# Performance work log

Measured on AMD Instinct MI355X. Metric: run time of the kernel, lower is better.

Reference implementation:

```python
import jax, jax.numpy as jnp
import numpy as np

TOP_K = 2

def setup_inputs() -> dict:
    key = jax.random.key(0)
    k1, k2, k3, k4 = jax.random.split(key, 4)
    B, S, H, E, F = 2, 1024, 1024, 16, 1024
    hidden_states = jax.random.normal(k1, (B, S, H), dtype=jnp.float32)
    router_w = jax.random.normal(k2, (H, E), dtype=jnp.float32) * 0.02
    w_gate_up = jax.random.normal(k3, (E, H, 2 * F), dtype=jnp.float32) * 0.02
    w_down = jax.random.normal(k4, (E, F, H), dtype=jnp.float32) * 0.02
    return {"hidden_states": hidden_states, "router_w": router_w,
            "w_gate_up": w_gate_up, "w_down": w_down}

def reference(hidden_states, router_w, w_gate_up, w_down):
    B, S, H = hidden_states.shape
    E = router_w.shape[-1]
    flat = hidden_states.reshape(-1, H)                      # [T, H]
    T = flat.shape[0]
    # Routing: topk_then_softmax (default softmax_order)
    logits = flat @ router_w                                 # [T, E]
    top_vals, top_idx = jax.lax.top_k(logits, TOP_K)         # [T, K]
    routing_weights = jax.nn.softmax(top_vals, axis=-1)      # [T, K]
    # Scatter routing weights into a dense combine matrix [T, E]
    combine = jnp.zeros((T, E), dtype=flat.dtype)
    combine = combine.at[jnp.arange(T)[:, None], top_idx].add(routing_weights)
    # Fused expert FFN (per _FusedExpertTemplate, act_fn = SiLU-gated)
    gu = jnp.einsum('th,ehf->etf', flat, w_gate_up)          # [E, T, 2F]
    gate, up = jnp.split(gu, 2, axis=-1)
    gated = jax.nn.silu(gate) * up                           # [E, T, F]
    expert_out = jnp.einsum('etf,efh->eth', gated, w_down)   # [E, T, H]
    out = jnp.einsum('eth,te->th', expert_out, combine)      # [T, H]
    return out.reshape(B, S, H)
```

## Files before the change

### kernel.cpp

```cpp
#include <hip/hip_runtime.h>

#define T_TOK 2048
#define H_DIM 1024
#define E_NUM 16
#define F_DIM 1024
#define NKB 32

typedef unsigned short u16;
typedef unsigned int u32;
typedef short s16x8 __attribute__((ext_vector_type(8)));
typedef float f32x4 __attribute__((ext_vector_type(4)));

__device__ __forceinline__ float b2f(u16 v) { return __uint_as_float(((u32)v) << 16); }
__device__ __forceinline__ u16 f2b(float f) {
  u32 u = __float_as_uint(f);
  return (u16)((u + 0x7fffu + ((u >> 16) & 1u)) >> 16);
}

__device__ __forceinline__ void gl_lds16(const u32* g, u32* l) {
  __builtin_amdgcn_global_load_lds((const __attribute__((address_space(1))) void*)g,
                                   (__attribute__((address_space(3))) void*)l, 16, 0, 0);
}

__global__ void router_kernel(const float* __restrict__ hidden, const float* __restrict__ rw,
                              int* __restrict__ counts, int* __restrict__ routing_e,
                              float* __restrict__ routing_w) {
  int t = blockIdx.x;
  int lane = threadIdx.x;
  const float* xrow = hidden + (size_t)t * H_DIM;
  float acc[E_NUM];
#pragma unroll
  for (int e = 0; e < E_NUM; ++e) acc[e] = 0.f;
  for (int j = 0; j < H_DIM / 64; ++j) {
    int h = j * 64 + lane;
    float x = xrow[h];
    const float* wr = rw + h * E_NUM;
#pragma unroll
    for (int e = 0; e < E_NUM; ++e) acc[e] += x * wr[e];
  }
#pragma unroll
  for (int e = 0; e < E_NUM; ++e) {
    acc[e] += __shfl_xor(acc[e], 32, 64);
    acc[e] += __shfl_xor(acc[e], 16, 64);
    acc[e] += __shfl_xor(acc[e], 8, 64);
    acc[e] += __shfl_xor(acc[e], 4, 64);
    acc[e] += __shfl_xor(acc[e], 2, 64);
    acc[e] += __shfl_xor(acc[e], 1, 64);
  }
  if (lane == 0) {
    float v0 = -1e30f, v1 = -1e30f;
    int i0 = 0, i1 = 0;
#pragma unroll
    for (int e = 0; e < E_NUM; ++e) {
      float v = acc[e];
      if (v > v0) { v1 = v0; i1 = i0; v0 = v; i0 = e; }
      else if (v > v1) { v1 = v; i1 = e; }
    }
    float p0 = 1.f / (1.f + __expf(v1 - v0));
    routing_e[2 * t] = i0;
    routing_e[2 * t + 1] = i1;
    routing_w[2 * t] = p0;
    routing_w[2 * t + 1] = 1.f - p0;
    atomicAdd(&counts[i0], 1);
    atomicAdd(&counts[i1], 1);
  }
}

__global__ void scatter_kernel(const int* __restrict__ counts, int* __restrict__ offsets,
                               const int* __restrict__ routing_e, const float* __restrict__ routing_w,
                               int* __restrict__ token_of_slot, float* __restrict__ slot_w) {
  __shared__ int offs[E_NUM];
  __shared__ int cur[E_NUM];
  int tid = threadIdx.x;
  if (tid == 0) {
    int s = 0;
    for (int e = 0; e < E_NUM; ++e) { offs[e] = s; s += counts[e]; }
  }
  __syncthreads();
  if (tid < E_NUM) { offsets[tid] = offs[tid]; cur[tid] = offs[tid]; }
  __syncthreads();
  for (int i = tid; i < 2 * T_TOK; i += 256) {
    int e = routing_e[i];
    int pos = atomicAdd(&cur[e], 1);
    token_of_slot[pos] = i >> 1;
    slot_w[pos] = routing_w[i];
  }
}

__device__ __forceinline__ void split_pack(const float* __restrict__ p, uint4& hh, uint4& ll) {
  u16 h[8], l[8];
#pragma unroll
  for (int i = 0; i < 8; ++i) {
    h[i] = f2b(p[i]);
    l[i] = f2b(p[i] - b2f(h[i]));
  }
  hh.x = (u32)h[0] | ((u32)h[1] << 16);
  hh.y = (u32)h[2] | ((u32)h[3] << 16);
  hh.z = (u32)h[4] | ((u32)h[5] << 16);
  hh.w = (u32)h[6] | ((u32)h[7] << 16);
  ll.x = (u32)l[0] | ((u32)l[1] << 16);
  ll.y = (u32)l[2] | ((u32)l[3] << 16);
  ll.z = (u32)l[4] | ((u32)l[5] << 16);
  ll.w = (u32)l[6] | ((u32)l[7] << 16);
}

__global__ __launch_bounds__(256) void prep_x(const float* __restrict__ x, u16* __restrict__ xh,
                                              u16* __restrict__ xl) {
  int i = blockIdx.x * 256 + threadIdx.x;
  float4 a = ((const float4*)x)[2 * i];
  float4 b = ((const float4*)x)[2 * i + 1];
  float v[8] = {a.x, a.y, a.z, a.w, b.x, b.y, b.z, b.w};
  uint4 hh, ll;
  split_pack(v, hh, ll);
  ((uint4*)xh)[i] = hh;
  ((uint4*)xl)[i] = ll;
}

__global__ __launch_bounds__(256) void prep_w(const float* __restrict__ w, u32* __restrict__ wt,
                                              int N) {
  const int e = blockIdx.z, nbk = blockIdx.y, kb = blockIdx.x;
  const float* src = w + (size_t)e * 1024 * N + (size_t)kb * 32 * N + nbk * 128;
  u32* dst = wt + (((size_t)e * gridDim.y + nbk) * NKB + kb) * 2048;
  __shared__ u16 L[32][132];
  const int t = threadIdx.x;
  const int kr = t >> 5;
  const int nq = (t & 31) * 4;
#pragma unroll
  for (int p = 0; p < 4; ++p) {
    int k = p * 8 + kr;
    float4 v = *(const float4*)(src + (size_t)k * N + nq);
    L[k][nq] = f2b(v.x);
    L[k][nq + 1] = f2b(v.y);
    L[k][nq + 2] = f2b(v.z);
    L[k][nq + 3] = f2b(v.w);
  }
  __syncthreads();
  const int n = t >> 1, half = t & 1;
  const int s = ((n >> 3) ^ n) & 3;
  __align__(16) u32 buf[8];
#pragma unroll
  for (int j = 0; j < 8; ++j) {
    int pos = half * 8 + j;
    int g0 = ((pos >> 2) ^ s) & 3;
    int kp = g0 * 4 + (pos & 3);
    buf[j] = (u32)L[2 * kp][n] | ((u32)L[2 * kp + 1][n] << 16);
  }
  *(uint4*)(dst + n * 16 + half * 8) = *(uint4*)&buf[0];
  *(uint4*)(dst + n * 16 + half * 8 + 4) = *(uint4*)&buf[4];
}

__device__ __forceinline__ s16x8 read_bfrag(const u32* __restrict__ B, int n, int q) {
  return *(const s16x8*)&B[n * 16 + (((q ^ (n >> 3) ^ n) & 3) << 2)];
}

#define MFMA(a, b, c) __builtin_amdgcn_mfma_f32_16x16x32_bf16(a, b, c, 0, 0, 0)

__global__ __launch_bounds__(256, 2) void moe_gemm1(
    const u16* __restrict__ Xh, const u16* __restrict__ Xl, const u32* __restrict__ wgu_t,
    const int* __restrict__ token_of_slot, const int* __restrict__ counts,
    const int* __restrict__ offsets, u16* __restrict__ act_h, u16* __restrict__ act_l) {
  const int e = blockIdx.z;
  const int cnt = counts[e];
  const int m0 = blockIdx.y * 64;
  if (m0 >= cnt) return;
  const int off = offsets[e];
  const int xb = blockIdx.x;

  __shared__ u32 Bg[2][2048];
  __shared__ u32 Bu[2][2048];

  const int tid = threadIdx.x;
  const int lane = tid & 63;
  const int wv = tid >> 6;
  const int q = lane >> 4, ln = lane & 15;
  const int mb = (wv & 1) * 32, nb = (wv >> 1) * 64;

  const int r0 = m0 + mb + ln, r1 = r0 + 16;
  const int t0 = (r0 < cnt) ? token_of_slot[off + r0] : 0;
  const int t1 = (r1 < cnt) ? token_of_slot[off + r1] : 0;
  const u16* xh0 = Xh + (size_t)t0 * H_DIM + q * 8;
  const u16* xh1 = Xh + (size_t)t1 * H_DIM + q * 8;
  const u16* xl0 = Xl + (size_t)t0 * H_DIM + q * 8;
  const u16* xl1 = Xl + (size_t)t1 * H_DIM + q * 8;

  const u32* g_g = wgu_t + (((size_t)e * 16 + xb) * NKB) * 2048 + tid * 4;
  const u32* g_u = wgu_t + (((size_t)e * 16 + xb + 8) * NKB) * 2048 + tid * 4;

  f32x4 zero = {0.f, 0.f, 0.f, 0.f};
  f32x4 accg[2][4], accu[2][4];
#pragma unroll
  for (int i = 0; i < 2; ++i)
#pragma unroll
    for (int j = 0; j < 4; ++j) { accg[i][j] = zero; accu[i][j] = zero; }

#define STAGE1(kbn, LG, LU)                          \
  {                                                  \
    const u32* sg = g_g + (size_t)(kbn) * 2048;      \
    const u32* su = g_u + (size_t)(kbn) * 2048;      \
    gl_lds16(sg, (LG) + wv * 256);                   \
    gl_lds16(sg + 1024, (LG) + 1024 + wv * 256);     \
    gl_lds16(su, (LU) + wv * 256);                   \
    gl_lds16(su + 1024, (LU) + 1024 + wv * 256);     \
  }

  STAGE1(0, &Bg[0][0], &Bu[0][0]);
  __syncthreads();

#define G1BODY(kb, CG, CU, NG, NU)                               \
  {                                                              \
    const int koff = (kb) * 32;                                  \
    s16x8 ah0 = *(const s16x8*)(xh0 + koff);                     \
    s16x8 ah1 = *(const s16x8*)(xh1 + koff);                     \
    s16x8 al0 = *(const s16x8*)(xl0 + koff);                     \
    s16x8 al1 = *(const s16x8*)(xl1 + koff);                     \
    if ((kb) + 1 < NKB) STAGE1((kb) + 1, NG, NU);                \
    _Pragma("unroll")                                            \
    for (int j = 0; j < 4; ++j) {                                \
      s16x8 bg = read_bfrag(CG, nb + j * 16 + ln, q);            \
      s16x8 bu = read_bfrag(CU, nb + j * 16 + ln, q);            \
      accg[0][j] = MFMA(ah0, bg, accg[0][j]);                    \
      accg[1][j] = MFMA(ah1, bg, accg[1][j]);                    \
      accu[0][j] = MFMA(ah0, bu, accu[0][j]);                    \
      accu[1][j] = MFMA(ah1, bu, accu[1][j]);                    \
      accg[0][j] = MFMA(al0, bg, accg[0][j]);                    \
      accg[1][j] = MFMA(al1, bg, accg[1][j]);                    \
      accu[0][j] = MFMA(al0, bu, accu[0][j]);                    \
      accu[1][j] = MFMA(al1, bu, accu[1][j]);                    \
    }                                                            \
    __syncthreads();                                             \
  }

  for (int kb = 0; kb < NKB; kb += 2) {
    G1BODY(kb, &Bg[0][0], &Bu[0][0], &Bg[1][0], &Bu[1][0]);
    G1BODY(kb + 1, &Bg[1][0], &Bu[1][0], &Bg[0][0], &Bu[0][0]);
  }

  const int bcol = xb * 128 + nb + ln;
#pragma unroll
  for (int i = 0; i < 2; ++i) {
#pragma unroll
    for (int r = 0; r < 4; ++r) {
      int row = mb + i * 16 + q * 4 + r;
      if (m0 + row < cnt) {
        size_t rb = (size_t)(off + m0 + row) * F_DIM + bcol;
#pragma unroll
        for (int j = 0; j < 4; ++j) {
          float g = accg[i][j][r], u = accu[i][j][r];
          float a = g * (1.f / (1.f + __expf(-g))) * u;
          u16 h = f2b(a);
          u16 l = f2b(a - b2f(h));
          act_h[rb + j * 16] = h;
          act_l[rb + j * 16] = l;
        }
      }
    }
  }
}

__global__ __launch_bounds__(256, 2) void moe_gemm2(
    const u16* __restrict__ Ah, const u16* __restrict__ Al, const u32* __restrict__ wd_t,
    const int* __restrict__ token_of_slot, const float* __restrict__ slot_w,
    const int* __restrict__ counts, const int* __restrict__ offsets,
    float* __restrict__ out) {
  const int e = blockIdx.z;
  const int cnt = counts[e];
  const int m0 = blockIdx.y * 64;
  if (m0 >= cnt) return;
  const int off = offsets[e];
  const int xb = blockIdx.x;

  __shared__ u32 Bd[2][2048];

  const int tid = threadIdx.x;
  const int lane = tid & 63;
  const int wv = tid >> 6;
  const int q = lane >> 4, ln = lane & 15;
  const int mb = (wv & 1) * 32, nb = (wv >> 1) * 64;

  const int r0 = m0 + mb + ln, r1 = r0 + 16;
  const int s0 = off + ((r0 < cnt) ? r0 : 0);
  const int s1 = off + ((r1 < cnt) ? r1 : 0);
  const u16* ah0 = Ah + (size_t)s0 * F_DIM + q * 8;
  const u16* ah1 = Ah + (size_t)s1 * F_DIM + q * 8;
  const u16* al0 = Al + (size_t)s0 * F_DIM + q * 8;
  const u16* al1 = Al + (size_t)s1 * F_DIM + q * 8;

  const u32* g_d = wd_t + (((size_t)e * 8 + xb) * NKB) * 2048 + tid * 4;

  f32x4 zero = {0.f, 0.f, 0.f, 0.f};
  f32x4 acc[2][4];
#pragma unroll
  for (int i = 0; i < 2; ++i)
#pragma unroll
    for (int j = 0; j < 4; ++j) acc[i][j] = zero;

#define STAGE2(kbn, LD)                              \
  {                                                  \
    const u32* sd = g_d + (size_t)(kbn) * 2048;      \
    gl_lds16(sd, (LD) + wv * 256);                   \
    gl_lds16(sd + 1024, (LD) + 1024 + wv * 256);     \
  }

  STAGE2(0, &Bd[0][0]);
  __syncthreads();

#define G2BODY(kb, CD, ND)                               \
  {                                                      \
    const int koff = (kb) * 32;                          \
    s16x8 a0 = *(const s16x8*)(ah0 + koff);              \
    s16x8 a1 = *(const s16x8*)(ah1 + koff);              \
    s16x8 b0 = *(const s16x8*)(al0 + koff);              \
    s16x8 b1 = *(const s16x8*)(al1 + koff);              \
    if ((kb) + 1 < NKB) STAGE2((kb) + 1, ND);            \
    _Pragma("unroll")                                    \
    for (int j = 0; j < 4; ++j) {                        \
      s16x8 bf = read_bfrag(CD, nb + j * 16 + ln, q);    \
      acc[0][j] = MFMA(a0, bf, acc[0][j]);               \
      acc[1][j] = MFMA(a1, bf, acc[1][j]);               \
      acc[0][j] = MFMA(b0, bf, acc[0][j]);               \
      acc[1][j] = MFMA(b1, bf, acc[1][j]);               \
    }                                                    \
    __syncthreads();                                     \
  }

  for (int kb = 0; kb < NKB; kb += 2) {
    G2BODY(kb, &Bd[0][0], &Bd[1][0]);
    G2BODY(kb + 1, &Bd[1][0], &Bd[0][0]);
  }

#pragma unroll
  for (int i = 0; i < 2; ++i) {
#pragma unroll
    for (int r = 0; r < 4; ++r) {
      int row = mb + i * 16 + q * 4 + r;
      if (m0 + row < cnt) {
        int slot = off + m0 + row;
        int tok = token_of_slot[slot];
        float wgt = slot_w[slot];
        float* orow = out + (size_t)tok * H_DIM + xb * 128 + nb + ln;
#pragma unroll
        for (int j = 0; j < 4; ++j) atomicAdd(&orow[j * 16], wgt * acc[i][j][r]);
      }
    }
  }
}

extern "C" void kernel_launch(void* const* d_in, const int* in_sizes, int n_in,
                              void* d_out, int out_size, void* d_ws, size_t ws_size,
                              hipStream_t stream) {
  const float* hidden = (const float*)d_in[0];
  const float* rw = (const float*)d_in[1];
  const float* wgu = (const float*)d_in[2];
  const float* wd = (const float*)d_in[3];
  float* out = (float*)d_out;
  char* ws = (char*)d_ws;

  int* counts = (int*)(ws);
  int* offsets = (int*)(ws + 256);
  int* routing_e = (int*)(ws + 1024);
  float* routing_w = (float*)(ws + 17408);
  int* token_of_slot = (int*)(ws + 33792);
  float* slot_w = (float*)(ws + 50176);
  u16* Xh = (u16*)(ws + 131072ull);
  u16* Xl = (u16*)(ws + 4325376ull);
  u16* act_h = (u16*)(ws + 8519680ull);
  u16* act_l = (u16*)(ws + 16908288ull);
  u32* wgu_t = (u32*)(ws + 25296896ull);
  u32* wd_t  = (u32*)(ws + 92405760ull);

  hipMemsetAsync(counts, 0, 64, stream);
  hipMemsetAsync(out, 0, (size_t)out_size * sizeof(float), stream);
  router_kernel<<<dim3(T_TOK), dim3(64), 0, stream>>>(hidden, rw, counts, routing_e, routing_w);
  scatter_kernel<<<dim3(1), dim3(256), 0, stream>>>(counts, offsets, routing_e, routing_w,
                                                    token_of_slot, slot_w);
  prep_x<<<dim3(T_TOK * H_DIM / 8 / 256), dim3(256), 0, stream>>>(hidden, Xh, Xl);
  prep_w<<<dim3(NKB, 16, E_NUM), dim3(256), 0, stream>>>(wgu, wgu_t, 2048);
  prep_w<<<dim3(NKB, 8, E_NUM), dim3(256), 0, stream>>>(wd, wd_t, 1024);
  moe_gemm1<<<dim3(8, 32, E_NUM), dim3(256), 0, stream>>>(Xh, Xl, wgu_t, token_of_slot, counts,
                                                          offsets, act_h, act_l);
  moe_gemm2<<<dim3(8, 32, E_NUM), dim3(256), 0, stream>>>(act_h, act_l, wd_t, token_of_slot,
                                                          slot_w, counts, offsets, out);
}
```

Before: 479.9 us.

## Deepen GEMM LDS pipelines, prefetch A fragments, restructure router and weight prep

Both expert GEMMs move from a double-buffered LDS pipeline to a four-slot ring with three stages in flight. They use explicit vmcnt waits and raw s_barrier instead of __syncthreads, prefetch the next A fragments into registers, and raise MFMA priority with s_setprio. gemm2 occupancy hint goes to 3 blocks. The router transposes the router weights so each expert's reads coalesce and packs 4 tokens per 256-thread block, and prep_w drops its LDS staging for direct strided column loads. These aim to hide global-load latency and cut barrier stalls, at the cost of more LDS per block (possible occupancy loss in gemm1) and fragile hand-tuned wait counts.

```diff
diff --git a/kernel.cpp b/kernel.cpp
--- a/kernel.cpp
+++ b/kernel.cpp
@@ -22,11 +22,20 @@
                                    (__attribute__((address_space(3))) void*)l, 16, 0, 0);
 }
 
-__global__ void router_kernel(const float* __restrict__ hidden, const float* __restrict__ rw,
-                              int* __restrict__ counts, int* __restrict__ routing_e,
-                              float* __restrict__ routing_w) {
-  int t = blockIdx.x;
-  int lane = threadIdx.x;
+__global__ __launch_bounds__(256) void rw_transpose_kernel(const float* __restrict__ rw,
+                                                           float* __restrict__ rwT) {
+  int idx = blockIdx.x * 256 + threadIdx.x;
+  float v = rw[idx];
+  rwT[(idx & 15) * 1024 + (idx >> 4)] = v;
+}
+
+__global__ __launch_bounds__(256) void router_kernel(const float* __restrict__ hidden,
+                                                     const float* __restrict__ rwT,
+                                                     int* __restrict__ counts,
+                                                     int* __restrict__ routing_e,
+                                                     float* __restrict__ routing_w) {
+  int wv = threadIdx.x >> 6, lane = threadIdx.x & 63;
+  int t = blockIdx.x * 4 + wv;
   const float* xrow = hidden + (size_t)t * H_DIM;
   float acc[E_NUM];
 #pragma unroll
@@ -34,9 +43,8 @@
   for (int j = 0; j < H_DIM / 64; ++j) {
     int h = j * 64 + lane;
     float x = xrow[h];
-    const float* wr = rw + h * E_NUM;
-#pragma unroll
-    for (int e = 0; e < E_NUM; ++e) acc[e] += x * wr[e];
+#pragma unroll
+    for (int e = 0; e < E_NUM; ++e) acc[e] += x * rwT[e * 1024 + h];
   }
 #pragma unroll
   for (int e = 0; e < E_NUM; ++e) {
@@ -121,32 +129,19 @@
   const int e = blockIdx.z, nbk = blockIdx.y, kb = blockIdx.x;
   const float* src = w + (size_t)e * 1024 * N + (size_t)kb * 32 * N + nbk * 128;
   u32* dst = wt + (((size_t)e * gridDim.y + nbk) * NKB + kb) * 2048;
-  __shared__ u16 L[32][132];
   const int t = threadIdx.x;
-  const int kr = t >> 5;
-  const int nq = (t & 31) * 4;
-#pragma unroll
-  for (int p = 0; p < 4; ++p) {
-    int k = p * 8 + kr;
-    float4 v = *(const float4*)(src + (size_t)k * N + nq);
-    L[k][nq] = f2b(v.x);
-    L[k][nq + 1] = f2b(v.y);
-    L[k][nq + 2] = f2b(v.z);
-    L[k][nq + 3] = f2b(v.w);
-  }
-  __syncthreads();
-  const int n = t >> 1, half = t & 1;
+  const int n = t & 127, h = t >> 7;
   const int s = ((n >> 3) ^ n) & 3;
-  __align__(16) u32 buf[8];
-#pragma unroll
-  for (int j = 0; j < 8; ++j) {
-    int pos = half * 8 + j;
-    int g0 = ((pos >> 2) ^ s) & 3;
-    int kp = g0 * 4 + (pos & 3);
-    buf[j] = (u32)L[2 * kp][n] | ((u32)L[2 * kp + 1][n] << 16);
-  }
-  *(uint4*)(dst + n * 16 + half * 8) = *(uint4*)&buf[0];
-  *(uint4*)(dst + n * 16 + half * 8 + 4) = *(uint4*)&buf[4];
+  const float* col = src + (size_t)(16 * h) * N + n;
+  float v[16];
+#pragma unroll
+  for (int kk = 0; kk < 16; ++kk) v[kk] = col[(size_t)kk * N];
+  __align__(16) u32 wbuf[8];
+#pragma unroll
+  for (int j = 0; j < 8; ++j) wbuf[j] = (u32)f2b(v[2 * j]) | ((u32)f2b(v[2 * j + 1]) << 16);
+  u32* row = dst + n * 16;
+  *(uint4*)(row + (((2 * h) ^ s) & 3) * 4) = *(uint4*)&wbuf[0];
+  *(uint4*)(row + (((2 * h + 1) ^ s) & 3) * 4) = *(uint4*)&wbuf[4];
 }
 
 __device__ __forceinline__ s16x8 read_bfrag(const u32* __restrict__ B, int n, int q) {
@@ -166,8 +161,8 @@
   const int off = offsets[e];
   const int xb = blockIdx.x;
 
-  __shared__ u32 Bg[2][2048];
-  __shared__ u32 Bu[2][2048];
+  __shared__ u32 Bg[4][2048];
+  __shared__ u32 Bu[4][2048];
 
   const int tid = threadIdx.x;
   const int lane = tid & 63;
@@ -193,47 +188,67 @@
 #pragma unroll
     for (int j = 0; j < 4; ++j) { accg[i][j] = zero; accu[i][j] = zero; }
 
-#define STAGE1(kbn, LG, LU)                          \
-  {                                                  \
-    const u32* sg = g_g + (size_t)(kbn) * 2048;      \
-    const u32* su = g_u + (size_t)(kbn) * 2048;      \
-    gl_lds16(sg, (LG) + wv * 256);                   \
-    gl_lds16(sg + 1024, (LG) + 1024 + wv * 256);     \
-    gl_lds16(su, (LU) + wv * 256);                   \
-    gl_lds16(su + 1024, (LU) + 1024 + wv * 256);     \
-  }
-
-  STAGE1(0, &Bg[0][0], &Bu[0][0]);
-  __syncthreads();
-
-#define G1BODY(kb, CG, CU, NG, NU)                               \
-  {                                                              \
-    const int koff = (kb) * 32;                                  \
-    s16x8 ah0 = *(const s16x8*)(xh0 + koff);                     \
-    s16x8 ah1 = *(const s16x8*)(xh1 + koff);                     \
-    s16x8 al0 = *(const s16x8*)(xl0 + koff);                     \
-    s16x8 al1 = *(const s16x8*)(xl1 + koff);                     \
-    if ((kb) + 1 < NKB) STAGE1((kb) + 1, NG, NU);                \
-    _Pragma("unroll")                                            \
-    for (int j = 0; j < 4; ++j) {                                \
-      s16x8 bg = read_bfrag(CG, nb + j * 16 + ln, q);            \
-      s16x8 bu = read_bfrag(CU, nb + j * 16 + ln, q);            \
-      accg[0][j] = MFMA(ah0, bg, accg[0][j]);                    \
-      accg[1][j] = MFMA(ah1, bg, accg[1][j]);                    \
-      accu[0][j] = MFMA(ah0, bu, accu[0][j]);                    \
-      accu[1][j] = MFMA(ah1, bu, accu[1][j]);                    \
-      accg[0][j] = MFMA(al0, bg, accg[0][j]);                    \
-      accg[1][j] = MFMA(al1, bg, accg[1][j]);                    \
-      accu[0][j] = MFMA(al0, bu, accu[0][j]);                    \
-      accu[1][j] = MFMA(al1, bu, accu[1][j]);                    \
-    }                                                            \
-    __syncthreads();                                             \
-  }
-
-  for (int kb = 0; kb < NKB; kb += 2) {
-    G1BODY(kb, &Bg[0][0], &Bu[0][0], &Bg[1][0], &Bu[1][0]);
-    G1BODY(kb + 1, &Bg[1][0], &Bu[1][0], &Bg[0][0], &Bu[0][0]);
-  }
+#define G1STAGE(KBN)                                      \
+  {                                                       \
+    const int bix = (KBN) & 3;                            \
+    const u32* sg = g_g + (size_t)(KBN) * 2048;           \
+    const u32* su = g_u + (size_t)(KBN) * 2048;           \
+    gl_lds16(sg, &Bg[bix][0] + wv * 256);                 \
+    gl_lds16(sg + 1024, &Bg[bix][0] + 1024 + wv * 256);   \
+    gl_lds16(su, &Bu[bix][0] + wv * 256);                 \
+    gl_lds16(su + 1024, &Bu[bix][0] + 1024 + wv * 256);   \
+  }
+
+  s16x8 pH0, pH1, pL0, pL1, qH0, qH1, qL0, qL1;
+
+  G1STAGE(0);
+  pH0 = *(const s16x8*)(xh0);
+  pH1 = *(const s16x8*)(xh1);
+  pL0 = *(const s16x8*)(xl0);
+  pL1 = *(const s16x8*)(xl1);
+  G1STAGE(1);
+  G1STAGE(2);
+
+#define G1BODY(KB, H0, H1, L0, L1, NH0, NH1, NL0, NL1, WN, DOPF, DOST)  \
+  {                                                                     \
+    if (DOPF) {                                                         \
+      const int ko = ((KB) + 1) * 32;                                   \
+      NH0 = *(const s16x8*)(xh0 + ko);                                  \
+      NH1 = *(const s16x8*)(xh1 + ko);                                  \
+      NL0 = *(const s16x8*)(xl0 + ko);                                  \
+      NL1 = *(const s16x8*)(xl1 + ko);                                  \
+    }                                                                   \
+    asm volatile("s_waitcnt vmcnt(" WN ")" ::: "memory");               \
+    __builtin_amdgcn_sched_barrier(0);                                  \
+    __builtin_amdgcn_s_barrier();                                       \
+    __builtin_amdgcn_sched_barrier(0);                                  \
+    if (DOST) G1STAGE((KB) + 3);                                        \
+    const u32* Bgc = &Bg[(KB) & 3][0];                                  \
+    const u32* Buc = &Bu[(KB) & 3][0];                                  \
+    __builtin_amdgcn_s_setprio(1);                                      \
+    _Pragma("unroll") for (int j = 0; j < 4; ++j) {                     \
+      s16x8 bg = read_bfrag(Bgc, nb + j * 16 + ln, q);                  \
+      s16x8 bu = read_bfrag(Buc, nb + j * 16 + ln, q);                  \
+      accg[0][j] = MFMA(H0, bg, accg[0][j]);                            \
+      accg[1][j] = MFMA(H1, bg, accg[1][j]);                            \
+      accu[0][j] = MFMA(H0, bu, accu[0][j]);                            \
+      accu[1][j] = MFMA(H1, bu, accu[1][j]);                            \
+      accg[0][j] = MFMA(L0, bg, accg[0][j]);                            \
+      accg[1][j] = MFMA(L1, bg, accg[1][j]);                            \
+      accu[0][j] = MFMA(L0, bu, accu[0][j]);                            \
+      accu[1][j] = MFMA(L1, bu, accu[1][j]);                            \
+    }                                                                   \
+    __builtin_amdgcn_s_setprio(0);                                      \
+  }
+
+  for (int kb = 0; kb < 28; kb += 2) {
+    G1BODY(kb, pH0, pH1, pL0, pL1, qH0, qH1, qL0, qL1, "8", 1, 1);
+    G1BODY(kb + 1, qH0, qH1, qL0, qL1, pH0, pH1, pL0, pL1, "8", 1, 1);
+  }
+  G1BODY(28, pH0, pH1, pL0, pL1, qH0, qH1, qL0, qL1, "8", 1, 1);
+  G1BODY(29, qH0, qH1, qL0, qL1, pH0, pH1, pL0, pL1, "8", 1, 0);
+  G1BODY(30, pH0, pH1, pL0, pL1, qH0, qH1, qL0, qL1, "4", 1, 0);
+  G1BODY(31, qH0, qH1, qL0, qL1, pH0, pH1, pL0, pL1, "0", 0, 0);
 
   const int bcol = xb * 128 + nb + ln;
 #pragma unroll
@@ -257,7 +272,7 @@
   }
 }
 
-__global__ __launch_bounds__(256, 2) void moe_gemm2(
+__global__ __launch_bounds__(256, 3) void moe_gemm2(
     const u16* __restrict__ Ah, const u16* __restrict__ Al, const u32* __restrict__ wd_t,
     const int* __restrict__ token_of_slot, const float* __restrict__ slot_w,
     const int* __restrict__ counts, const int* __restrict__ offsets,
@@ -269,7 +284,7 @@
   const int off = offsets[e];
   const int xb = blockIdx.x;
 
-  __shared__ u32 Bd[2][2048];
+  __shared__ u32 Bd[4][2048];
 
   const int tid = threadIdx.x;
   const int lane = tid & 63;
@@ -294,39 +309,58 @@
 #pragma unroll
     for (int j = 0; j < 4; ++j) acc[i][j] = zero;
 
-#define STAGE2(kbn, LD)                              \
-  {                                                  \
-    const u32* sd = g_d + (size_t)(kbn) * 2048;      \
-    gl_lds16(sd, (LD) + wv * 256);                   \
-    gl_lds16(sd + 1024, (LD) + 1024 + wv * 256);     \
-  }
-
-  STAGE2(0, &Bd[0][0]);
-  __syncthreads();
-
-#define G2BODY(kb, CD, ND)                               \
-  {                                                      \
-    const int koff = (kb) * 32;                          \
-    s16x8 a0 = *(const s16x8*)(ah0 + koff);              \
-    s16x8 a1 = *(const s16x8*)(ah1 + koff);              \
-    s16x8 b0 = *(const s16x8*)(al0 + koff);              \
-    s16x8 b1 = *(const s16x8*)(al1 + koff);              \
-    if ((kb) + 1 < NKB) STAGE2((kb) + 1, ND);            \
-    _Pragma("unroll")                                    \
-    for (int j = 0; j < 4; ++j) {                        \
-      s16x8 bf = read_bfrag(CD, nb + j * 16 + ln, q);    \
-      acc[0][j] = MFMA(a0, bf, acc[0][j]);               \
-      acc[1][j] = MFMA(a1, bf, acc[1][j]);               \
-      acc[0][j] = MFMA(b0, bf, acc[0][j]);               \
-      acc[1][j] = MFMA(b1, bf, acc[1][j]);               \
-    }                                                    \
-    __syncthreads();                                     \
-  }
-
-  for (int kb = 0; kb < NKB; kb += 2) {
-    G2BODY(kb, &Bd[0][0], &Bd[1][0]);
-    G2BODY(kb + 1, &Bd[1][0], &Bd[0][0]);
-  }
+#define G2STAGE(KBN)                                      \
+  {                                                       \
+    const int bix = (KBN) & 3;                            \
+    const u32* sd = g_d + (size_t)(KBN) * 2048;           \
+    gl_lds16(sd, &Bd[bix][0] + wv * 256);                 \
+    gl_lds16(sd + 1024, &Bd[bix][0] + 1024 + wv * 256);   \
+  }
+
+  s16x8 pH0, pH1, pL0, pL1, qH0, qH1, qL0, qL1;
+
+  G2STAGE(0);
+  pH0 = *(const s16x8*)(ah0);
+  pH1 = *(const s16x8*)(ah1);
+  pL0 = *(const s16x8*)(al0);
+  pL1 = *(const s16x8*)(al1);
+  G2STAGE(1);
+  G2STAGE(2);
+
+#define G2BODY(KB, H0, H1, L0, L1, NH0, NH1, NL0, NL1, WN, DOPF, DOST)  \
+  {                                                                     \
+    if (DOPF) {                                                         \
+      const int ko = ((KB) + 1) * 32;                                   \
+      NH0 = *(const s16x8*)(ah0 + ko);                                  \
+      NH1 = *(const s16x8*)(ah1 + ko);                                  \
+      NL0 = *(const s16x8*)(al0 + ko);                                  \
+      NL1 = *(const s16x8*)(al1 + ko);                                  \
+    }                                                                   \
+    asm volatile("s_waitcnt vmcnt(" WN ")" ::: "memory");               \
+    __builtin_amdgcn_sched_barrier(0);                                  \
+    __builtin_amdgcn_s_barrier();                                       \
+    __builtin_amdgcn_sched_barrier(0);                                  \
+    if (DOST) G2STAGE((KB) + 3);                                        \
+    const u32* Bdc = &Bd[(KB) & 3][0];                                  \
+    __builtin_amdgcn_s_setprio(1);                                      \
+    _Pragma("unroll") for (int j = 0; j < 4; ++j) {                     \
+      s16x8 bf = read_bfrag(Bdc, nb + j * 16 + ln, q);                  \
+      acc[0][j] = MFMA(H0, bf, acc[0][j]);                              \
+      acc[1][j] = MFMA(H1, bf, acc[1][j]);                              \
+      acc[0][j] = MFMA(L0, bf, acc[0][j]);                              \
+      acc[1][j] = MFMA(L1, bf, acc[1][j]);                              \
+    }                                                                   \
+    __builtin_amdgcn_s_setprio(0);                                      \
+  }
+
+  for (int kb = 0; kb < 28; kb += 2) {
+    G2BODY(kb, pH0, pH1, pL0, pL1, qH0, qH1, qL0, qL1, "6", 1, 1);
+    G2BODY(kb + 1, qH0, qH1, qL0, qL1, pH0, pH1, pL0, pL1, "6", 1, 1);
+  }
+  G2BODY(28, pH0, pH1, pL0, pL1, qH0, qH1, qL0, qL1, "6", 1, 1);
+  G2BODY(29, qH0, qH1, qL0, qL1, pH0, pH1, pL0, pL1, "6", 1, 0);
+  G2BODY(30, pH0, pH1, pL0, pL1, qH0, qH1, qL0, qL1, "4", 1, 0);
+  G2BODY(31, qH0, qH1, qL0, qL1, pH0, pH1, pL0, pL1, "0", 0, 0);
 
 #pragma unroll
   for (int i = 0; i < 2; ++i) {
@@ -361,6 +395,7 @@
   float* routing_w = (float*)(ws + 17408);
   int* token_of_slot = (int*)(ws + 33792);
   float* slot_w = (float*)(ws + 50176);
+  float* rwT = (float*)(ws + 65536);
   u16* Xh = (u16*)(ws + 131072ull);
   u16* Xl = (u16*)(ws + 4325376ull);
   u16* act_h = (u16*)(ws + 8519680ull);
@@ -370,7 +405,9 @@
 
   hipMemsetAsync(counts, 0, 64, stream);
   hipMemsetAsync(out, 0, (size_t)out_size * sizeof(float), stream);
-  router_kernel<<<dim3(T_TOK), dim3(64), 0, stream>>>(hidden, rw, counts, routing_e, routing_w);
+  rw_transpose_kernel<<<dim3(64), dim3(256), 0, stream>>>(rw, rwT);
+  router_kernel<<<dim3(T_TOK / 4), dim3(256), 0, stream>>>(hidden, rwT, counts, routing_e,
+                                                           routing_w);
   scatter_kernel<<<dim3(1), dim3(256), 0, stream>>>(counts, offsets, routing_e, routing_w,
                                                     token_of_slot, slot_w);
   prep_x<<<dim3(T_TOK * H_DIM / 8 / 256), dim3(256), 0, stream>>>(hidden, Xh, Xl);
```

Measured after the change: 490.0 us. 2.1% more time.
